# Kernel optimization log

Hardware: AMD Instinct MI355X
Metric: run time of the kernel (lower is better)

The kernel has to match this reference:

```python
import jax, jax.numpy as jnp
import numpy as np
from jax import lax

B, T = 16384, 10
CAR, REG, POI, WEEK, TIME = 500000, 10000, 64, 7, 1440
H, LBL = 256, 512


def setup_inputs() -> dict:
    key = jax.random.key(0)
    ks = jax.random.split(key, 32)
    p = lambda i, shp: jax.random.normal(ks[i], shp, jnp.float32) * 0.05
    d = {}
    d["region_idx"] = jax.random.randint(ks[0], (B, T), 0, REG)
    d["poi_idx"] = jax.random.randint(ks[1], (B, T), 0, POI)
    d["car_idx"] = jax.random.randint(ks[2], (B,), 0, CAR)
    d["week_idx"] = jax.random.randint(ks[3], (B,), 0, WEEK)
    d["time_idx"] = jax.random.randint(ks[4], (B,), 0, TIME)
    d["coords"] = jax.random.normal(ks[5], (B, T, 2), jnp.float32)
    d["region_tbl"] = p(6, (REG, 8))
    d["poi_tbl"] = p(7, (POI, 4))
    d["car_tbl"] = p(8, (CAR, 16))
    d["week_tbl"] = p(9, (WEEK, 3))
    d["time_tbl"] = p(10, (TIME, 8))
    d["W_rp"] = p(11, (12, 32)); d["b_rp"] = p(12, (32,))
    d["W_co"] = p(13, (2, 8));  d["b_co"] = p(14, (8,))
    d["conv_w"] = p(15, (3, 40, 32)); d["conv_b"] = p(16, (32,))
    # 2-layer LSTM (torch gate order i,f,g,o), input 59, hidden 256
    d["Wih0"] = p(17, (4 * H, 59)); d["Whh0"] = p(18, (4 * H, H))
    d["bih0"] = p(19, (4 * H,));    d["bhh0"] = p(20, (4 * H,))
    d["Wih1"] = p(21, (4 * H, H)); d["Whh1"] = p(22, (4 * H, H))
    d["bih1"] = p(23, (4 * H,));   d["bhh1"] = p(24, (4 * H,))
    d["W1"] = p(25, (H, 512));    d["b1"] = p(26, (512,))
    d["W2"] = p(27, (512, 1024)); d["b2"] = p(28, (1024,))
    d["W3"] = p(29, (1024, LBL)); d["b3"] = p(30, (LBL,))
    return d


def _lstm_layer(x, Wih, Whh, bih, bhh):
    Bx, Hh = x.shape[0], Whh.shape[1]
    bias = bih + bhh

    def step(carry, xt):
        h, c = carry
        g = xt @ Wih.T + h @ Whh.T + bias
        i, f, gg, o = jnp.split(g, 4, axis=-1)
        c = jax.nn.sigmoid(f) * c + jax.nn.sigmoid(i) * jnp.tanh(gg)
        h = jax.nn.sigmoid(o) * jnp.tanh(c)
        return (h, c), h

    h0 = jnp.zeros((Bx, Hh), x.dtype)
    _, hs = lax.scan(step, (h0, h0), jnp.swapaxes(x, 0, 1))
    return jnp.swapaxes(hs, 0, 1)


def reference(region_idx, poi_idx, car_idx, week_idx, time_idx, coords,
              region_tbl, poi_tbl, car_tbl, week_tbl, time_tbl,
              W_rp, b_rp, W_co, b_co, conv_w, conv_b,
              Wih0, Whh0, bih0, bhh0, Wih1, Whh1, bih1, bhh1,
              W1, b1, W2, b2, W3, b3):
    # batched embedding gathers (replaces per-item python-loop lookups)
    rp = jnp.concatenate([region_tbl[region_idx], poi_tbl[poi_idx]], -1)   # [B,T,12]
    nv = jnp.concatenate([rp @ W_rp + b_rp, coords @ W_co + b_co], -1)     # [B,T,40]
    conv = jax.nn.elu(
        lax.conv_general_dilated(nv, conv_w, (1,), 'VALID',
                                 dimension_numbers=('NWC', 'WIO', 'NWC')) + conv_b)  # [B,T-2,32]
    emb = jnp.tanh(jnp.concatenate(
        [car_tbl[car_idx], week_tbl[week_idx], time_tbl[time_idx]], -1))   # [B,27]
    x = jnp.concatenate(
        [conv, jnp.broadcast_to(emb[:, None, :], conv.shape[:2] + (27,))], -1)  # [B,T-2,59]
    h = _lstm_layer(x, Wih0, Whh0, bih0, bhh0)
    h = _lstm_layer(h, Wih1, Whh1, bih1, bhh1)
    last = h[:, -1, :]                                                     # [B,256]
    # nn.Sequential of three Linears with NO activations between
    return ((last @ W1 + b1) @ W2 + b2) @ W3 + b3                          # [B,LBL]
```

## Files before the change

### kernel.cpp

```cpp
#include <hip/hip_runtime.h>
#include <hip/hip_bf16.h>
#include <math.h>

#define B_SZ 16384
#define T_CONV 8
#define HID 256
#define SK 16

typedef __bf16 bf16x8 __attribute__((ext_vector_type(8)));
typedef float f32x4 __attribute__((ext_vector_type(4)));

__device__ __forceinline__ float fsigm(float x) { return 1.f / (1.f + __expf(-x)); }
__device__ __forceinline__ float ftanh(float x) {
    float t = __expf(-2.f * fabsf(x));
    float r = (1.f - t) / (1.f + t);
    return x >= 0.f ? r : -r;
}

__global__ void collapse_conv(const float* __restrict__ W_rp, const float* __restrict__ b_rp,
                              const float* __restrict__ W_co, const float* __restrict__ b_co,
                              const float* __restrict__ conv_w, const float* __restrict__ conv_b,
                              float* __restrict__ Crp, float* __restrict__ Cco,
                              float* __restrict__ cb2)
{
    int idx = blockIdx.x * 256 + threadIdx.x;
    if (idx < 1152) {
        int o = idx & 31, k = (idx >> 5) % 12, dt = idx / 384;
        float a = 0.f;
        for (int c = 0; c < 32; c++) a += W_rp[k * 32 + c] * conv_w[(dt * 40 + c) * 32 + o];
        Crp[idx] = a;
    } else if (idx < 1344) {
        int j = idx - 1152;
        int o = j & 31, k = (j >> 5) & 1, dt = j / 64;
        float a = 0.f;
        for (int c = 0; c < 8; c++) a += W_co[k * 8 + c] * conv_w[(dt * 40 + 32 + c) * 32 + o];
        Cco[j] = a;
    } else if (idx < 1376) {
        int o = idx - 1344;
        float a = conv_b[o];
        for (int dt = 0; dt < 3; dt++) {
            for (int c = 0; c < 32; c++) a += b_rp[c] * conv_w[(dt * 40 + c) * 32 + o];
            for (int c = 0; c < 8; c++)  a += b_co[c] * conv_w[(dt * 40 + 32 + c) * 32 + o];
        }
        cb2[o] = a;
    }
}

#define FB_SAMPLES 4
__global__ __launch_bounds__(256) void feature_kernel(
    const int* __restrict__ region_idx, const int* __restrict__ poi_idx,
    const int* __restrict__ car_idx, const int* __restrict__ week_idx,
    const int* __restrict__ time_idx, const float* __restrict__ coords,
    const float* __restrict__ region_tbl, const float* __restrict__ poi_tbl,
    const float* __restrict__ car_tbl, const float* __restrict__ week_tbl,
    const float* __restrict__ time_tbl,
    const float* __restrict__ Crp, const float* __restrict__ Cco,
    const float* __restrict__ cb2, __bf16* __restrict__ Xp)
{
    __shared__ float s_crp[1152];
    __shared__ float s_cco[192];
    __shared__ float s_cb2[32];
    __shared__ float s_rp[FB_SAMPLES][10][12];
    __shared__ float s_co[FB_SAMPLES][10][2];
    __shared__ float s_emb[FB_SAMPLES][27];

    int tid = threadIdx.x;
    for (int i = tid; i < 1152; i += 256) s_crp[i] = Crp[i];
    if (tid < 192) s_cco[tid] = Cco[tid];
    else if (tid < 224) s_cb2[tid - 192] = cb2[tid - 192];

    int s  = tid >> 6;
    int lt = tid & 63;
    int b  = blockIdx.x * FB_SAMPLES + s;

    if (lt < 27) {
        float v;
        if (lt < 16)      v = car_tbl[(size_t)car_idx[b] * 16 + lt];
        else if (lt < 19) v = week_tbl[week_idx[b] * 3 + (lt - 16)];
        else              v = time_tbl[time_idx[b] * 8 + (lt - 19)];
        s_emb[s][lt] = tanhf(v);
    }
    for (int i = lt; i < 120; i += 64) {
        int t = i / 12, k = i % 12;
        float v;
        if (k < 8) v = region_tbl[(size_t)region_idx[b * 10 + t] * 8 + k];
        else       v = poi_tbl[poi_idx[b * 10 + t] * 4 + (k - 8)];
        s_rp[s][t][k] = v;
    }
    for (int i = lt; i < 20; i += 64) {
        int t = i >> 1, k = i & 1;
        s_co[s][t][k] = coords[(size_t)(b * 10 + t) * 2 + k];
    }
    __syncthreads();

    for (int i = lt; i < 256; i += 64) {
        int t = i >> 5, o = i & 31;
        float acc = s_cb2[o];
        #pragma unroll
        for (int dt = 0; dt < 3; dt++) {
            #pragma unroll
            for (int k = 0; k < 12; k++)
                acc += s_rp[s][t + dt][k] * s_crp[(dt * 12 + k) * 32 + o];
            acc += s_co[s][t + dt][0] * s_cco[(dt * 2 + 0) * 32 + o]
                 + s_co[s][t + dt][1] * s_cco[(dt * 2 + 1) * 32 + o];
        }
        acc = acc > 0.f ? acc : expm1f(acc);
        Xp[(size_t)(b * 8 + t) * 64 + o] = (__bf16)acc;
    }
    for (int i = lt; i < 216; i += 64) {
        int t = i / 27, j = i % 27;
        Xp[(size_t)(b * 8 + t) * 64 + 32 + j] = (__bf16)s_emb[s][j];
    }
    for (int i = lt; i < 40; i += 64) {
        int t = i / 5, j = i % 5;
        Xp[(size_t)(b * 8 + t) * 64 + 59 + j] = (__bf16)0.f;
    }
}

#define AST 40
__device__ __forceinline__ void lstm_body(
    unsigned char* smem,
    const __bf16* __restrict__ A1, int lda1, int K1,
    const __bf16* __restrict__ A2, int lda2,
    const __bf16* __restrict__ WS,
    const float* __restrict__ bias, float* __restrict__ cst,
    __bf16* __restrict__ hb,
    int KT, int is_t0)
{
    __bf16* As = (__bf16*)smem;
    float*  GL = (float*)smem;

    int tid = threadIdx.x;
    int bm  = blockIdx.y * 64;
    int bnf = blockIdx.x * 4;
    int bn  = blockIdx.x * 64;
    int l   = tid & 63;
    int g   = tid >> 6;
    int fr  = l & 15;
    int fo  = (l >> 4) * 8;

    f32x4 acc[4][4] = {};

    int s_row = tid >> 2;
    int s_q   = tid & 3;

    auto asrc = [&](int kt) -> const __bf16* {
        int k0 = kt * 32;
        if (k0 < K1) return A1 + (size_t)(bm + s_row) * lda1 + k0 + s_q * 8;
        return A2 + (size_t)(bm + s_row) * lda2 + (k0 - K1) + s_q * 8;
    };
    const __bf16* wbase = WS + ((size_t)g * 16 + bnf) * 512 + (size_t)l * 8;

    { *(bf16x8*)&As[s_row * AST + s_q * 8] = *(const bf16x8*)asrc(0); }
    bf16x8 bcur[4];
    #pragma unroll
    for (int j = 0; j < 4; j++) bcur[j] = *(const bf16x8*)(wbase + j * 512);

    for (int kt = 0; kt < KT; kt++) {
        int cb = kt & 1;
        bf16x8 bnxt[4], an0;
        if (kt + 1 < KT) {
            an0 = *(const bf16x8*)asrc(kt + 1);
            const __bf16* wb = wbase + (size_t)(kt + 1) * 32768;
            #pragma unroll
            for (int j = 0; j < 4; j++) bnxt[j] = *(const bf16x8*)(wb + j * 512);
        }
        __syncthreads();
        bf16x8 af[4];
        #pragma unroll
        for (int mf = 0; mf < 4; mf++)
            af[mf] = *(bf16x8*)&As[cb * 64 * AST + (mf * 16 + fr) * AST + fo];
        #pragma unroll
        for (int mf = 0; mf < 4; mf++)
            #pragma unroll
            for (int j = 0; j < 4; j++)
                acc[mf][j] = __builtin_amdgcn_mfma_f32_16x16x32_bf16(
                    af[mf], bcur[j], acc[mf][j], 0, 0, 0);
        if (kt + 1 < KT) {
            *(bf16x8*)&As[(cb ^ 1) * 64 * AST + s_row * AST + s_q * 8] = an0;
            #pragma unroll
            for (int j = 0; j < 4; j++) bcur[j] = bnxt[j];
        }
    }

    int rbase = (l >> 4) * 4;
    int prow  = tid >> 4;
    int pcol  = (tid & 15) * 4;
    f32x4 bs[4];
    #pragma unroll
    for (int gg = 0; gg < 4; gg++)
        bs[gg] = *(const f32x4*)&bias[gg * 256 + bn + pcol];

    #pragma unroll
    for (int mf = 0; mf < 4; mf++) {
        __syncthreads();
        #pragma unroll
        for (int j = 0; j < 4; j++)
            #pragma unroll
            for (int e = 0; e < 4; e++)
                GL[(g * 16 + rbase + e) * 68 + j * 16 + fr] = acc[mf][j][e];
        __syncthreads();

        size_t moff = ((size_t)bm + mf * 16 + prow) * 256 + bn + pcol;
        f32x4 gi = *(f32x4*)&GL[(0 * 16 + prow) * 68 + pcol];
        f32x4 gf = *(f32x4*)&GL[(1 * 16 + prow) * 68 + pcol];
        f32x4 gg = *(f32x4*)&GL[(2 * 16 + prow) * 68 + pcol];
        f32x4 go = *(f32x4*)&GL[(3 * 16 + prow) * 68 + pcol];
        f32x4 cold = {0.f, 0.f, 0.f, 0.f};
        if (!is_t0) cold = *(f32x4*)&cst[moff];
        f32x4 cn;
        union { unsigned short u[4]; unsigned long long v; } hx;
        #pragma unroll
        for (int q = 0; q < 4; q++) {
            float i_ = fsigm(gi[q] + bs[0][q]);
            float f_ = fsigm(gf[q] + bs[1][q]);
            float g_ = ftanh(gg[q] + bs[2][q]);
            float o_ = fsigm(go[q] + bs[3][q]);
            float c_ = f_ * cold[q] + i_ * g_;
            cn[q] = c_;
            float h_ = o_ * ftanh(c_);
            __bf16 hv = (__bf16)h_;
            hx.u[q] = *(unsigned short*)&hv;
        }
        *(f32x4*)&cst[moff] = cn;
        *(unsigned long long*)&hb[moff] = hx.v;
    }
}

__global__ __launch_bounds__(256, 2) void lstm_fused(
    const __bf16* __restrict__ A1, int lda1, int K1,
    const __bf16* __restrict__ A2, int lda2,
    const __bf16* __restrict__ WS,
    const float* __restrict__ bias, float* __restrict__ cst,
    __bf16* __restrict__ hb, int KT, int is_t0)
{
    __shared__ __align__(16) unsigned char smem[4 * 16 * 68 * 4];
    lstm_body(smem, A1, lda1, K1, A2, lda2, WS, bias, cst, hb, KT, is_t0);
}

__global__ __launch_bounds__(256, 2) void lstm_dual(
    const __bf16* A1a, int lda1a, int K1a, const __bf16* A2a, int lda2a,
    const __bf16* WSa, const float* biasa, float* csta, __bf16* hba, int KTa, int t0a,
    const __bf16* A1b, int lda1b, int K1b, const __bf16* A2b, int lda2b,
    const __bf16* WSb, const float* biasb, float* cstb, __bf16* hbb, int KTb, int t0b)
{
    __shared__ __align__(16) unsigned char smem[4 * 16 * 68 * 4];
    if (blockIdx.z == 0)
        lstm_body(smem, A1a, lda1a, K1a, A2a, lda2a, WSa, biasa, csta, hba, KTa, t0a);
    else
        lstm_body(smem, A1b, lda1b, K1b, A2b, lda2b, WSb, biasb, cstb, hbb, KTb, t0b);
}

#define HAST 40
__global__ __launch_bounds__(256, 2) void head_mfma(
    const __bf16* __restrict__ A,
    const __bf16* __restrict__ WS,
    const float* __restrict__ bias, float* __restrict__ out)
{
    __shared__ __align__(16) __bf16 As[2][128 * HAST];

    int tid = threadIdx.x;
    int bm  = blockIdx.y * 128;
    int l   = tid & 63;
    int wv  = tid >> 6;
    int fr  = l & 15;
    int fo  = (l >> 4) * 8;
    int nfb = blockIdx.x * 16 + wv * 4;

    f32x4 acc[8][4] = {};

    int s_row  = tid >> 1;
    int s_half = tid & 1;
    const __bf16* abase = A + (size_t)(bm + s_row) * 256 + s_half * 16;
    const __bf16* wbase = WS + (size_t)nfb * 512 + (size_t)l * 8;

    {
        bf16x8 v0 = *(const bf16x8*)abase;
        bf16x8 v1 = *(const bf16x8*)(abase + 8);
        *(bf16x8*)&As[0][s_row * HAST + s_half * 16]     = v0;
        *(bf16x8*)&As[0][s_row * HAST + s_half * 16 + 8] = v1;
    }
    bf16x8 bcur[4];
    #pragma unroll
    for (int j = 0; j < 4; j++) bcur[j] = *(const bf16x8*)(wbase + j * 512);

    #pragma unroll
    for (int kt = 0; kt < 8; kt++) {
        int cb = kt & 1;
        bf16x8 bnxt[4], an0, an1;
        if (kt + 1 < 8) {
            const __bf16* s = abase + (kt + 1) * 32;
            an0 = *(const bf16x8*)s;
            an1 = *(const bf16x8*)(s + 8);
            const __bf16* wb = wbase + (size_t)(kt + 1) * 16384;
            #pragma unroll
            for (int j = 0; j < 4; j++) bnxt[j] = *(const bf16x8*)(wb + j * 512);
        }
        __syncthreads();
        bf16x8 af[8];
        #pragma unroll
        for (int mf = 0; mf < 8; mf++)
            af[mf] = *(bf16x8*)&As[cb][(mf * 16 + fr) * HAST + fo];
        #pragma unroll
        for (int mf = 0; mf < 8; mf++)
            #pragma unroll
            for (int j = 0; j < 4; j++)
                acc[mf][j] = __builtin_amdgcn_mfma_f32_16x16x32_bf16(
                    af[mf], bcur[j], acc[mf][j], 0, 0, 0);
        if (kt + 1 < 8) {
            *(bf16x8*)&As[cb ^ 1][s_row * HAST + s_half * 16]     = an0;
            *(bf16x8*)&As[cb ^ 1][s_row * HAST + s_half * 16 + 8] = an1;
            #pragma unroll
            for (int j = 0; j < 4; j++) bcur[j] = bnxt[j];
        }
    }

    int rbase = (l >> 4) * 4;
    #pragma unroll
    for (int mf = 0; mf < 8; mf++) {
        #pragma unroll
        for (int j = 0; j < 4; j++) {
            int n = (nfb + j) * 16 + fr;
            float bv = bias[n];
            #pragma unroll
            for (int e = 0; e < 4; e++) {
                size_t m = (size_t)bm + mf * 16 + rbase + e;
                out[m * 512 + n] = acc[mf][j][e] + bv;
            }
        }
    }
}

__global__ __launch_bounds__(256) void gemm_nn_sk(
    const float* __restrict__ A, int lda, const float* __restrict__ Bm, int ldb,
    float* __restrict__ P, int M, int N, int K)
{
    __shared__ float As[16][68];
    __shared__ float Bs[16][68];
    int tid = threadIdx.x;
    int tx = tid & 15, ty = tid >> 4;
    int bm = blockIdx.y * 64, bn = blockIdx.x * 64;
    int klen = K / SK;
    int kbeg = blockIdx.z * klen;

    float acc[4][4] = {};

    for (int k0 = kbeg; k0 < kbeg + klen; k0 += 16) {
        for (int i = tid; i < 1024; i += 256) {
            int k = i & 15, m = i >> 4;
            As[k][m] = A[(size_t)(bm + m) * lda + k0 + k];
        }
        for (int i = tid; i < 1024; i += 256) {
            int n = i & 63, k = i >> 6;
            Bs[k][n] = Bm[(size_t)(k0 + k) * ldb + bn + n];
        }
        __syncthreads();
        #pragma unroll
        for (int kk = 0; kk < 16; kk++) {
            float4 a = *(const float4*)&As[kk][ty * 4];
            float4 b = *(const float4*)&Bs[kk][tx * 4];
            float av[4] = {a.x, a.y, a.z, a.w};
            float bv[4] = {b.x, b.y, b.z, b.w};
            #pragma unroll
            for (int i = 0; i < 4; i++)
                #pragma unroll
                for (int j = 0; j < 4; j++)
                    acc[i][j] += av[i] * bv[j];
        }
        __syncthreads();
    }

    float* Pd = P + (size_t)blockIdx.z * M * N;
    #pragma unroll
    for (int i = 0; i < 4; i++) {
        int m = bm + ty * 4 + i;
        #pragma unroll
        for (int j = 0; j < 4; j++) {
            int n = bn + tx * 4 + j;
            Pd[(size_t)m * N + n] = acc[i][j];
        }
    }
}

__global__ __launch_bounds__(256) void reduce_sk(
    const float* __restrict__ P, int MN, float* __restrict__ C)
{
    int i = blockIdx.x * 256 + threadIdx.x;
    if (i >= MN) return;
    float a = 0.f;
    #pragma unroll
    for (int s = 0; s < SK; s++) a += P[(size_t)s * MN + i];
    C[i] = a;
}

__global__ __launch_bounds__(256) void vecmat(
    const float* __restrict__ v, const float* __restrict__ M, int ldb, int K,
    const float* __restrict__ bias, float* __restrict__ outv)
{
    __shared__ float red[4][64];
    int l = threadIdx.x & 63;
    int w = threadIdx.x >> 6;
    int n = blockIdx.x * 64 + l;
    int kpw = K >> 2;
    int k0 = w * kpw;

    float p[8] = {};
    for (int k = k0; k < k0 + kpw; k += 8) {
        #pragma unroll
        for (int u = 0; u < 8; u++)
            p[u] += v[k + u] * M[(size_t)(k + u) * ldb + n];
    }
    red[w][l] = ((p[0] + p[1]) + (p[2] + p[3])) + ((p[4] + p[5]) + (p[6] + p[7]));
    __syncthreads();
    if (w == 0)
        outv[n] = red[0][l] + red[1][l] + red[2][l] + red[3][l]
                + (bias ? bias[n] : 0.f);
}

__global__ void add_biases(const float* __restrict__ bih0, const float* __restrict__ bhh0,
                           const float* __restrict__ bih1, const float* __restrict__ bhh1,
                           float* __restrict__ b01)
{
    int i = blockIdx.x * 256 + threadIdx.x;
    if (i < 1024)       b01[i] = bih0[i] + bhh0[i];
    else if (i < 2048)  b01[i] = bih1[i - 1024] + bhh1[i - 1024];
}

__global__ void pack_w01_swz(const float* __restrict__ Wih0, const float* __restrict__ Whh0,
                             const float* __restrict__ Wih1, const float* __restrict__ Whh1,
                             __bf16* __restrict__ WS0, __bf16* __restrict__ WS1)
{
    const int N0 = 10 * 4 * 16 * 64 * 8;
    const int N1 = 16 * 4 * 16 * 64 * 8;
    int idx = blockIdx.x * 256 + threadIdx.x;
    if (idx < N0) {
        int e  = idx & 7;
        int l  = (idx >> 3) & 63;
        int nf = (idx >> 9) & 15;
        int g  = (idx >> 13) & 3;
        int kt = idx >> 15;
        int n_row = g * 256 + nf * 16 + (l & 15);
        int k = kt * 32 + ((l >> 4) * 8) + e;
        float v = (k < 59) ? Wih0[(size_t)n_row * 59 + k]
                : (k < 64) ? 0.f
                           : Whh0[(size_t)n_row * 256 + (k - 64)];
        WS0[idx] = (__bf16)v;
    } else if (idx < N0 + N1) {
        int j = idx - N0;
        int e  = j & 7;
        int l  = (j >> 3) & 63;
        int nf = (j >> 9) & 15;
        int g  = (j >> 13) & 3;
        int kt = j >> 15;
        int n_row = g * 256 + nf * 16 + (l & 15);
        int k = kt * 32 + ((l >> 4) * 8) + e;
        float v = (k < 256) ? Wih1[(size_t)n_row * 256 + k]
                            : Whh1[(size_t)n_row * 256 + (k - 256)];
        WS1[j] = (__bf16)v;
    }
}

__global__ void pack_head_swz(const float* __restrict__ Wc, __bf16* __restrict__ WS)
{
    int idx = blockIdx.x * 256 + threadIdx.x;
    if (idx >= 8 * 32 * 64 * 8) return;
    int e  = idx & 7;
    int l  = (idx >> 3) & 63;
    int nf = (idx >> 9) & 31;
    int kt = idx >> 14;
    int n = nf * 16 + (l & 15);
    int k = kt * 32 + ((l >> 4) * 8) + e;
    WS[idx] = (__bf16)Wc[(size_t)k * 512 + n];
}

extern "C" void kernel_launch(void* const* d_in, const int* in_sizes, int n_in,
                              void* d_out, int out_size, void* d_ws, size_t ws_size,
                              hipStream_t stream)
{
    const int*   region_idx = (const int*)d_in[0];
    const int*   poi_idx    = (const int*)d_in[1];
    const int*   car_idx    = (const int*)d_in[2];
    const int*   week_idx   = (const int*)d_in[3];
    const int*   time_idx   = (const int*)d_in[4];
    const float* coords     = (const float*)d_in[5];
    const float* region_tbl = (const float*)d_in[6];
    const float* poi_tbl    = (const float*)d_in[7];
    const float* car_tbl    = (const float*)d_in[8];
    const float* week_tbl   = (const float*)d_in[9];
    const float* time_tbl   = (const float*)d_in[10];
    const float* W_rp   = (const float*)d_in[11];
    const float* b_rp   = (const float*)d_in[12];
    const float* W_co   = (const float*)d_in[13];
    const float* b_co   = (const float*)d_in[14];
    const float* conv_w = (const float*)d_in[15];
    const float* conv_b = (const float*)d_in[16];
    const float* Wih0 = (const float*)d_in[17];
    const float* Whh0 = (const float*)d_in[18];
    const float* bih0 = (const float*)d_in[19];
    const float* bhh0 = (const float*)d_in[20];
    const float* Wih1 = (const float*)d_in[21];
    const float* Whh1 = (const float*)d_in[22];
    const float* bih1 = (const float*)d_in[23];
    const float* bhh1 = (const float*)d_in[24];
    const float* W1 = (const float*)d_in[25];
    const float* b1 = (const float*)d_in[26];
    const float* W2 = (const float*)d_in[27];
    const float* b2 = (const float*)d_in[28];
    const float* W3 = (const float*)d_in[29];
    const float* b3 = (const float*)d_in[30];
    float* out = (float*)d_out;

    char* ws = (char*)d_ws;
    size_t off = 0;
    auto alloc = [&](size_t bytes) -> char* {
        char* p = ws + off;
        off = (off + bytes + 255) & ~(size_t)255;
        return p;
    };
    __bf16* Xp   = (__bf16*)alloc((size_t)B_SZ * 8 * 64 * 2);
    __bf16* H0a  = (__bf16*)alloc((size_t)B_SZ * HID * 2);
    __bf16* H0b  = (__bf16*)alloc((size_t)B_SZ * HID * 2);
    __bf16* H1a  = (__bf16*)alloc((size_t)B_SZ * HID * 2);
    __bf16* H1b  = (__bf16*)alloc((size_t)B_SZ * HID * 2);
    float*  c0   = (float*)alloc((size_t)B_SZ * HID * 4);
    float*  c1   = (float*)alloc((size_t)B_SZ * HID * 4);
    __bf16* WS0  = (__bf16*)alloc((size_t)10 * 4 * 16 * 64 * 8 * 2);
    __bf16* WS1  = (__bf16*)alloc((size_t)16 * 4 * 16 * 64 * 8 * 2);
    __bf16* WSH  = (__bf16*)alloc((size_t)8 * 32 * 64 * 8 * 2);
    float*  T1    = (float*)alloc(256 * 1024 * 4);
    float*  tb1   = (float*)alloc(1024 * 4);
    float*  Wcomb = (float*)alloc(256 * 512 * 4);
    float*  bcomb = (float*)alloc(512 * 4);
    float*  b01   = (float*)alloc(2048 * 4);
    float*  Crp   = (float*)alloc(1152 * 4);
    float*  Cco   = (float*)alloc(192 * 4);
    float*  cb2   = (float*)alloc(32 * 4);
    float*  Psk   = (float*)alloc((size_t)SK * 256 * 1024 * 4);
    (void)ws_size;
    float* bias0 = b01;
    float* bias1 = b01 + 1024;
    __bf16* H0[2] = {H0a, H0b};
    __bf16* H1[2] = {H1a, H1b};

    pack_w01_swz<<<3328, 256, 0, stream>>>(Wih0, Whh0, Wih1, Whh1, WS0, WS1);
    add_biases<<<8, 256, 0, stream>>>(bih0, bhh0, bih1, bhh1, b01);
    collapse_conv<<<6, 256, 0, stream>>>(W_rp, b_rp, W_co, b_co, conv_w, conv_b,
                                         Crp, Cco, cb2);

    gemm_nn_sk<<<dim3(16, 4, SK), 256, 0, stream>>>(W1, 512, W2, 1024, Psk, 256, 1024, 512);
    reduce_sk<<<(256 * 1024 + 255) / 256, 256, 0, stream>>>(Psk, 256 * 1024, T1);
    vecmat<<<16, 256, 0, stream>>>(b1, W2, 1024, 512, b2, tb1);
    gemm_nn_sk<<<dim3(8, 4, SK), 256, 0, stream>>>(T1, 1024, W3, 512, Psk, 256, 512, 1024);
    reduce_sk<<<(256 * 512 + 255) / 256, 256, 0, stream>>>(Psk, 256 * 512, Wcomb);
    vecmat<<<8, 256, 0, stream>>>(tb1, W3, 512, 1024, b3, bcomb);
    pack_head_swz<<<512, 256, 0, stream>>>(Wcomb, WSH);

    feature_kernel<<<B_SZ / FB_SAMPLES, 256, 0, stream>>>(
        region_idx, poi_idx, car_idx, week_idx, time_idx, coords,
        region_tbl, poi_tbl, car_tbl, week_tbl, time_tbl,
        Crp, Cco, cb2, Xp);

    dim3 lstm_grid(4, B_SZ / 64);
    dim3 dual_grid(4, B_SZ / 64, 2);

    lstm_fused<<<lstm_grid, 256, 0, stream>>>(
        Xp, 512, 64, H0[1], HID, WS0, bias0, c0, H0[0], 2, 1);

    for (int t = 0; t < T_CONV - 1; t++) {
        int pc = t & 1, pn = (t + 1) & 1;
        lstm_dual<<<dual_grid, 256, 0, stream>>>(
            H0[pc], HID, 256, H1[pn], HID, WS1, bias1, c1, H1[pc],
            (t == 0) ? 8 : 16, t == 0,
            Xp + (size_t)(t + 1) * 64, 512, 64, H0[pc], HID, WS0, bias0, c0, H0[pn],
            10, 0);
    }

    lstm_fused<<<lstm_grid, 256, 0, stream>>>(
        H0[1], HID, 256, H1[0], HID, WS1, bias1, c1, H1[1], 16, 0);

    head_mfma<<<dim3(2, 128), 256, 0, stream>>>(H1[1], WSH, bcomb, out);
}
```

Measured before the change: 502.5 us.

## Remap LSTM warp tiling so each wave holds all four gates in registers

Reassigns the four waves of the LSTM GEMM from one-gate-per-wave to a 2x2 split over rows and hidden columns, with each wave computing all four gates (i,f,g,o) for its tile. The gate nonlinearity and cell update can then run directly from the accumulator registers, dropping the shared-memory gate transpose, its per-fragment barriers, and most of the LDS footprint. The cost is more B-fragment loads per wave per k-step (8 instead of 4, while A fragments drop from 4 to 2), and scalar cst/hb global accesses with a strided pattern in place of the previous vectorized 4-wide stores.

Result: slower. 559.7 us (+11.4%).

```diff
diff --git a/kernel.cpp b/kernel.cpp
--- a/kernel.cpp
+++ b/kernel.cpp
@@ -119,7 +119,7 @@
 
 #define AST 40
 __device__ __forceinline__ void lstm_body(
-    unsigned char* smem,
+    __bf16* As,
     const __bf16* __restrict__ A1, int lda1, int K1,
     const __bf16* __restrict__ A2, int lda2,
     const __bf16* __restrict__ WS,
@@ -127,19 +127,18 @@
     __bf16* __restrict__ hb,
     int KT, int is_t0)
 {
-    __bf16* As = (__bf16*)smem;
-    float*  GL = (float*)smem;
-
     int tid = threadIdx.x;
     int bm  = blockIdx.y * 64;
     int bnf = blockIdx.x * 4;
     int bn  = blockIdx.x * 64;
     int l   = tid & 63;
-    int g   = tid >> 6;
+    int w   = tid >> 6;
+    int mh  = w & 1;
+    int nh  = w >> 1;
     int fr  = l & 15;
     int fo  = (l >> 4) * 8;
 
-    f32x4 acc[4][4] = {};
+    f32x4 acc[2][2][4] = {};
 
     int s_row = tid >> 2;
     int s_q   = tid & 3;
@@ -149,81 +148,75 @@
         if (k0 < K1) return A1 + (size_t)(bm + s_row) * lda1 + k0 + s_q * 8;
         return A2 + (size_t)(bm + s_row) * lda2 + (k0 - K1) + s_q * 8;
     };
-    const __bf16* wbase = WS + ((size_t)g * 16 + bnf) * 512 + (size_t)l * 8;
+    const __bf16* wbase = WS + (size_t)(bnf + nh * 2) * 512 + (size_t)l * 8;
 
     { *(bf16x8*)&As[s_row * AST + s_q * 8] = *(const bf16x8*)asrc(0); }
-    bf16x8 bcur[4];
-    #pragma unroll
-    for (int j = 0; j < 4; j++) bcur[j] = *(const bf16x8*)(wbase + j * 512);
+    bf16x8 bcur[2][4];
+    #pragma unroll
+    for (int nj = 0; nj < 2; nj++)
+        #pragma unroll
+        for (int g = 0; g < 4; g++)
+            bcur[nj][g] = *(const bf16x8*)(wbase + g * 8192 + nj * 512);
 
     for (int kt = 0; kt < KT; kt++) {
         int cb = kt & 1;
-        bf16x8 bnxt[4], an0;
+        bf16x8 bnxt[2][4], an0;
         if (kt + 1 < KT) {
             an0 = *(const bf16x8*)asrc(kt + 1);
-            const __bf16* wb = wbase + (size_t)(kt + 1) * 32768;
-            #pragma unroll
-            for (int j = 0; j < 4; j++) bnxt[j] = *(const bf16x8*)(wb + j * 512);
+            const __bf16* wbk = wbase + (size_t)(kt + 1) * 32768;
+            #pragma unroll
+            for (int nj = 0; nj < 2; nj++)
+                #pragma unroll
+                for (int g = 0; g < 4; g++)
+                    bnxt[nj][g] = *(const bf16x8*)(wbk + g * 8192 + nj * 512);
         }
         __syncthreads();
-        bf16x8 af[4];
-        #pragma unroll
-        for (int mf = 0; mf < 4; mf++)
-            af[mf] = *(bf16x8*)&As[cb * 64 * AST + (mf * 16 + fr) * AST + fo];
-        #pragma unroll
-        for (int mf = 0; mf < 4; mf++)
-            #pragma unroll
-            for (int j = 0; j < 4; j++)
-                acc[mf][j] = __builtin_amdgcn_mfma_f32_16x16x32_bf16(
-                    af[mf], bcur[j], acc[mf][j], 0, 0, 0);
+        bf16x8 af[2];
+        #pragma unroll
+        for (int mi = 0; mi < 2; mi++)
+            af[mi] = *(bf16x8*)&As[cb * 64 * AST + (mh * 32 + mi * 16 + fr) * AST + fo];
+        #pragma unroll
+        for (int mi = 0; mi < 2; mi++)
+            #pragma unroll
+            for (int nj = 0; nj < 2; nj++)
+                #pragma unroll
+                for (int g = 0; g < 4; g++)
+                    acc[mi][nj][g] = __builtin_amdgcn_mfma_f32_16x16x32_bf16(
+                        af[mi], bcur[nj][g], acc[mi][nj][g], 0, 0, 0);
         if (kt + 1 < KT) {
             *(bf16x8*)&As[(cb ^ 1) * 64 * AST + s_row * AST + s_q * 8] = an0;
             #pragma unroll
-            for (int j = 0; j < 4; j++) bcur[j] = bnxt[j];
+            for (int nj = 0; nj < 2; nj++)
+                #pragma unroll
+                for (int g = 0; g < 4; g++)
+                    bcur[nj][g] = bnxt[nj][g];
         }
     }
 
     int rbase = (l >> 4) * 4;
-    int prow  = tid >> 4;
-    int pcol  = (tid & 15) * 4;
-    f32x4 bs[4];
-    #pragma unroll
-    for (int gg = 0; gg < 4; gg++)
-        bs[gg] = *(const f32x4*)&bias[gg * 256 + bn + pcol];
-
-    #pragma unroll
-    for (int mf = 0; mf < 4; mf++) {
-        __syncthreads();
-        #pragma unroll
-        for (int j = 0; j < 4; j++)
-            #pragma unroll
-            for (int e = 0; e < 4; e++)
-                GL[(g * 16 + rbase + e) * 68 + j * 16 + fr] = acc[mf][j][e];
-        __syncthreads();
-
-        size_t moff = ((size_t)bm + mf * 16 + prow) * 256 + bn + pcol;
-        f32x4 gi = *(f32x4*)&GL[(0 * 16 + prow) * 68 + pcol];
-        f32x4 gf = *(f32x4*)&GL[(1 * 16 + prow) * 68 + pcol];
-        f32x4 gg = *(f32x4*)&GL[(2 * 16 + prow) * 68 + pcol];
-        f32x4 go = *(f32x4*)&GL[(3 * 16 + prow) * 68 + pcol];
-        f32x4 cold = {0.f, 0.f, 0.f, 0.f};
-        if (!is_t0) cold = *(f32x4*)&cst[moff];
-        f32x4 cn;
-        union { unsigned short u[4]; unsigned long long v; } hx;
-        #pragma unroll
-        for (int q = 0; q < 4; q++) {
-            float i_ = fsigm(gi[q] + bs[0][q]);
-            float f_ = fsigm(gf[q] + bs[1][q]);
-            float g_ = ftanh(gg[q] + bs[2][q]);
-            float o_ = fsigm(go[q] + bs[3][q]);
-            float c_ = f_ * cold[q] + i_ * g_;
-            cn[q] = c_;
-            float h_ = o_ * ftanh(c_);
-            __bf16 hv = (__bf16)h_;
-            hx.u[q] = *(unsigned short*)&hv;
-        }
-        *(f32x4*)&cst[moff] = cn;
-        *(unsigned long long*)&hb[moff] = hx.v;
+    #pragma unroll
+    for (int mi = 0; mi < 2; mi++) {
+        #pragma unroll
+        for (int nj = 0; nj < 2; nj++) {
+            int col = bn + nh * 32 + nj * 16 + fr;
+            float bi  = bias[col];
+            float bf_ = bias[256 + col];
+            float bg  = bias[512 + col];
+            float bo  = bias[768 + col];
+            #pragma unroll
+            for (int e = 0; e < 4; e++) {
+                int row = mh * 32 + mi * 16 + rbase + e;
+                size_t moff = ((size_t)bm + row) * 256 + col;
+                float cd = is_t0 ? 0.f : cst[moff];
+                float i_ = fsigm(acc[mi][nj][0][e] + bi);
+                float f_ = fsigm(acc[mi][nj][1][e] + bf_);
+                float g_ = ftanh(acc[mi][nj][2][e] + bg);
+                float o_ = fsigm(acc[mi][nj][3][e] + bo);
+                float c_ = f_ * cd + i_ * g_;
+                cst[moff] = c_;
+                hb[moff] = (__bf16)(o_ * ftanh(c_));
+            }
+        }
     }
 }
 
@@ -234,7 +227,7 @@
     const float* __restrict__ bias, float* __restrict__ cst,
     __bf16* __restrict__ hb, int KT, int is_t0)
 {
-    __shared__ __align__(16) unsigned char smem[4 * 16 * 68 * 4];
+    __shared__ __align__(16) __bf16 smem[2 * 64 * AST];
     lstm_body(smem, A1, lda1, K1, A2, lda2, WS, bias, cst, hb, KT, is_t0);
 }
 
@@ -244,7 +237,7 @@
     const __bf16* A1b, int lda1b, int K1b, const __bf16* A2b, int lda2b,
     const __bf16* WSb, const float* biasb, float* cstb, __bf16* hbb, int KTb, int t0b)
 {
-    __shared__ __align__(16) unsigned char smem[4 * 16 * 68 * 4];
+    __shared__ __align__(16) __bf16 smem[2 * 64 * AST];
     if (blockIdx.z == 0)
         lstm_body(smem, A1a, lda1a, K1a, A2a, lda2a, WSa, biasa, csta, hba, KTa, t0a);
     else
```
